# Kernel optimization log

Measured on AMD Instinct MI355X. Metric: run time of the kernel, lower is better.

## Reference

```python
import jax, jax.numpy as jnp
import numpy as np

N = 65536            # total nodes = B * NODES_PER_GRAPH
E = 524288           # edges (avg degree 8)
B = 64               # graphs per batch
NODES_PER_GRAPH = 1024
KS = 3               # SplineConv kernel_size per pseudo-dim
DEG = 2              # B-spline degree


def setup_inputs() -> dict:
    key = jax.random.key(0)
    ks = jax.random.split(key, 32)

    def w(k, shape, fan_in):
        return jax.random.normal(k, shape, jnp.float32) * (1.0 / np.sqrt(fan_in))

    inp = {
        "x": jax.random.normal(ks[0], (N, 16), jnp.float32),
        "edge_index": jax.random.randint(ks[1], (2, E), 0, N, jnp.int64),
        "pos": jax.random.uniform(ks[2], (E, 2), jnp.float32),  # pseudo-coords in [0,1]
        "batch": jnp.sort(jax.random.randint(ks[3], (N,), 0, B, jnp.int64)),
    }
    dims = [("enc0", 16, 32), ("enc1", 32, 64), ("enc2", 64, 64),
            ("dec0", 128, 64), ("dec1", 96, 32)]
    for i, (name, ci, co) in enumerate(dims):
        inp[name + "_W"] = w(ks[4 + 3 * i], (KS * KS, ci, co), ci * KS * KS)
        inp[name + "_root"] = w(ks[5 + 3 * i], (ci, co), ci)
        inp[name + "_b"] = jnp.zeros((co,), jnp.float32)
    inp["lin1_W"] = w(ks[20], (NODES_PER_GRAPH * 32, 128), NODES_PER_GRAPH * 32)
    inp["lin1_b"] = jnp.zeros((128,), jnp.float32)
    inp["lin2_W"] = w(ks[21], (128, 3), 128)
    inp["lin2_b"] = jnp.zeros((3,), jnp.float32)
    return inp


def _spline_basis(pseudo):
    """Open B-spline basis, degree 2, kernel_size 3, dim 2 (torch_spline_conv math).
    Returns basis [E, 9] and flattened weight indices [E, 9]."""
    v = pseudo * (KS - DEG)                    # scale to [0, ks-deg] = [0, 1]
    f = v - jnp.floor(v)                       # fractional part [E, 2]
    base = jnp.floor(v).astype(jnp.int32)
    # quadratic B-spline pieces for offsets s = 0, 1, 2
    b = jnp.stack([0.5 * (1.0 - f) ** 2, -f * f + f + 0.5, 0.5 * f * f], axis=-1)  # [E,2,3]
    idx = jnp.clip(base[..., None] + jnp.arange(3), 0, KS - 1)                      # [E,2,3]
    basis = (b[:, 0, :, None] * b[:, 1, None, :]).reshape(-1, 9)                    # [E,9]
    widx = (idx[:, 0, :, None] + KS * idx[:, 1, None, :]).reshape(-1, 9)            # [E,9]
    return basis, widx


def _spline_conv(x, src, dst, basis, widx, W, root, bias, n):
    """SplineConv: per-node transform under each of K kernels, then edge-wise
    basis-weighted gather, mean-scatter to targets, plus root linear + bias."""
    xW = jnp.einsum('ni,kio->nko', x, W)       # [N, 9, out]
    msg = basis[:, 0:1] * xW[src, widx[:, 0]]
    for s in range(1, 9):                      # fixed S = (deg+1)^2 = 9 taps
        msg = msg + basis[:, s:s + 1] * xW[src, widx[:, s]]
    agg = jax.ops.segment_sum(msg, dst, num_segments=n)
    deg = jax.ops.segment_sum(jnp.ones((msg.shape[0],), msg.dtype), dst, num_segments=n)
    out = agg / jnp.maximum(deg, 1.0)[:, None]  # mean aggregation (PyG default)
    return out + x @ root + bias


def _relu6(x):
    return jnp.clip(x, 0.0, 6.0)


def reference(x, edge_index, pos, batch,
              enc0_W, enc0_root, enc0_b,
              enc1_W, enc1_root, enc1_b,
              enc2_W, enc2_root, enc2_b,
              dec0_W, dec0_root, dec0_b,
              dec1_W, dec1_root, dec1_b,
              lin1_W, lin1_b, lin2_W, lin2_b):
    src, dst = edge_index[0], edge_index[1]
    basis, widx = _spline_basis(pos)
    n = x.shape[0]
    outs = [x]
    for W, R, bb in [(enc0_W, enc0_root, enc0_b),
                     (enc1_W, enc1_root, enc1_b),
                     (enc2_W, enc2_root, enc2_b)]:
        outs.append(_relu6(_spline_conv(outs[-1], src, dst, basis, widx, W, R, bb, n)))
    # decoder with skip-concat (encoder_bn/decoder_bn are never used in forward)
    d_in = jnp.concatenate([outs[3], outs[2]], axis=1)                 # 64+64 = 128
    dout = _relu6(_spline_conv(d_in, src, dst, basis, widx, dec0_W, dec0_root, dec0_b, n))
    d_in = jnp.concatenate([dout, outs[1]], axis=1)                    # 64+32 = 96
    dout = _relu6(_spline_conv(d_in, src, dst, basis, widx, dec1_W, dec1_root, dec1_b, n))
    flat = dout.reshape(B, NODES_PER_GRAPH * 32)                       # batch_size = max(batch)+1 = 64 (static)
    h = jax.nn.relu(flat @ lin1_W + lin1_b)
    return h @ lin2_W + lin2_b
```

## Files before the change

kernel.cpp:

```cpp
#include <hip/hip_runtime.h>

#define KS 3
#define NN 65536
#define EE 524288
#define BB 64

typedef unsigned short u16;
typedef unsigned int u32;

typedef __attribute__((ext_vector_type(8))) short bf16x8;
typedef __attribute__((ext_vector_type(4))) float f32x4;

__device__ __forceinline__ float bf2f(u16 u) {
  union { u32 i; float f; } v; v.i = ((u32)u) << 16; return v.f;
}
__device__ __forceinline__ u16 f2bf(float f) {
  union { float f; u32 i; } v; v.f = f;
  u32 x = v.i;
  x += 0x7fffu + ((x >> 16) & 1u);
  return (u16)(x >> 16);
}

static const size_t O_CR   = 0;
static const size_t O_ROWS = 10485760;
static const size_t O_CURS = 10748160;
static const size_t O_BSUM = 11010304;
static const size_t O_BMAT = 11011328;
static const size_t O_XB   = 11379968;
static const size_t O_H1   = 13477184;
static const size_t O_H2   = 17671488;
static const size_t O_H3   = 26060096;
static const size_t O_D0   = 34448704;
static const size_t O_D1   = 42837312;
static const size_t O_HBUF = 47031616;
static const size_t O_DEG  = 47064384;

__global__ void cvt_x(const float* __restrict__ x, u16* __restrict__ xb) {
  int i = blockIdx.x * 256 + threadIdx.x;
  xb[i] = f2bf(x[i]);
}

__global__ void hist_kernel(const int* __restrict__ ei, int* __restrict__ deg) {
  int e = blockIdx.x * 256 + threadIdx.x;
  int d = ei[EE + e]; d = min(max(d, 0), NN - 1);
  atomicAdd(&deg[d], 1);
}

__global__ void scan1(const int* __restrict__ deg, int* __restrict__ rows,
                      int* __restrict__ bsum) {
  __shared__ int s[256];
  int t = threadIdx.x, b = blockIdx.x, i = b * 256 + t;
  int v = deg[i];
  s[t] = v; __syncthreads();
  for (int off = 1; off < 256; off <<= 1) {
    int x = (t >= off) ? s[t - off] : 0; __syncthreads();
    s[t] += x; __syncthreads();
  }
  rows[i] = s[t] - v;
  if (t == 255) bsum[b] = s[255];
}
__global__ void scan2(int* __restrict__ bsum) {
  __shared__ int s[256];
  int t = threadIdx.x;
  int v = bsum[t];
  s[t] = v; __syncthreads();
  for (int off = 1; off < 256; off <<= 1) {
    int x = (t >= off) ? s[t - off] : 0; __syncthreads();
    s[t] += x; __syncthreads();
  }
  bsum[t] = s[t] - v;
}
__global__ void scan3(int* __restrict__ rows, const int* __restrict__ bsum,
                      int* __restrict__ cursor) {
  int t = threadIdx.x, b = blockIdx.x, i = b * 256 + t;
  int v = rows[i] + bsum[b];
  rows[i] = v;
  cursor[i] = v;
  if (i == NN - 1) rows[NN] = EE;
}

__global__ void fill_kernel(const int* __restrict__ ei, const float* __restrict__ pos,
                            int* __restrict__ cursor, u32* __restrict__ cr) {
  int e = blockIdx.x * 256 + threadIdx.x;
  int src = ei[e];      src = min(max(src, 0), NN - 1);
  int dst = ei[EE + e]; dst = min(max(dst, 0), NN - 1);
  float2 p = ((const float2*)pos)[e];
  float fl0 = floorf(p.x), fl1 = floorf(p.y);
  float f0 = p.x - fl0, f1 = p.y - fl1;
  int b0 = (int)fl0, b1 = (int)fl1;
  float w0[3] = { 0.5f*(1.f-f0)*(1.f-f0), -f0*f0+f0+0.5f, 0.5f*f0*f0 };
  float w1[3] = { 0.5f*(1.f-f1)*(1.f-f1), -f1*f1+f1+0.5f, 0.5f*f1*f1 };
  int i0[3], i1[3];
#pragma unroll
  for (int s = 0; s < 3; ++s) {
    i0[s] = min(max(b0 + s, 0), KS - 1);
    i1[s] = min(max(b1 + s, 0), KS - 1);
  }
  float c[9] = {0,0,0,0,0,0,0,0,0};
#pragma unroll
  for (int s0 = 0; s0 < 3; ++s0)
#pragma unroll
    for (int s1 = 0; s1 < 3; ++s1)
      c[i0[s0] + KS * i1[s1]] += w0[s0] * w1[s1];
  u16 h[9];
#pragma unroll
  for (int k = 0; k < 9; ++k) h[k] = f2bf(c[k]);
  int slot = atomicAdd(&cursor[dst], 1);
  slot = min(max(slot, 0), EE - 1);
  size_t b = (size_t)slot * 5;
  cr[b + 0] = (u32)(u16)src | ((u32)h[0] << 16);
  cr[b + 1] = (u32)h[1] | ((u32)h[2] << 16);
  cr[b + 2] = (u32)h[3] | ((u32)h[4] << 16);
  cr[b + 3] = (u32)h[5] | ((u32)h[6] << 16);
  cr[b + 4] = (u32)h[7] | ((u32)h[8] << 16);
}

struct BDesc { const float* W; int dstOff, i0, INW, OUT, K, isRoot; };
struct BDescs { BDesc d[18]; };

__global__ void build_b(BDescs ds, u16* __restrict__ bmat) {
  BDesc d = ds.d[blockIdx.y];
  int idx = blockIdx.x * 256 + threadIdx.x;
  int elems = d.K * d.OUT;
  if (idx >= elems) return;
  int o = idx / d.K, r = idx - o * d.K;
  float v;
  if (d.isRoot) {
    v = (r < d.INW) ? d.W[(size_t)(d.i0 + r) * d.OUT + o] : 0.f;
  } else {
    int kk = r >> 5, ii = r & 31;
    int i = d.i0 + ii;
    v = (i < d.INW) ? d.W[((size_t)kk * d.INW + i) * d.OUT + o] : 0.f;
  }
  bmat[(size_t)d.dstOff + (size_t)o * d.K + r] = f2bf(v);
}

struct PD { const u16* src; const u16* src2; int IN, IN2, mode, bOffA, ncA, bOffB, ncB; };
struct RD { const u16* src; int astride, ksteps, bOff; };
struct FArgs { PD ch; RD rt[2]; int nrt; const float* bias; u16* dst; };

#define NSTRIDE 1192

#define DECODE9U(Q0)                                              \
    u32 q1 = __builtin_amdgcn_readfirstlane(p[1]);                \
    u32 q2 = __builtin_amdgcn_readfirstlane(p[2]);                \
    u32 q3 = __builtin_amdgcn_readfirstlane(p[3]);                \
    u32 q4 = __builtin_amdgcn_readfirstlane(p[4]);                \
    float c0 = bf2f((u16)((Q0) >> 16));                           \
    float c1 = bf2f((u16)(q1 & 0xffffu)), c2 = bf2f((u16)(q1 >> 16)); \
    float c3 = bf2f((u16)(q2 & 0xffffu)), c4 = bf2f((u16)(q2 >> 16)); \
    float c5 = bf2f((u16)(q3 & 0xffffu)), c6 = bf2f((u16)(q3 >> 16)); \
    float c7 = bf2f((u16)(q4 & 0xffffu)), c8 = bf2f((u16)(q4 >> 16));

#define DECODE9V(Q0)                                              \
    u32 q1 = p[1], q2 = p[2], q3 = p[3], q4 = p[4];               \
    float c0 = bf2f((u16)((Q0) >> 16));                           \
    float c1 = bf2f((u16)(q1 & 0xffffu)), c2 = bf2f((u16)(q1 >> 16)); \
    float c3 = bf2f((u16)(q2 & 0xffffu)), c4 = bf2f((u16)(q2 >> 16)); \
    float c5 = bf2f((u16)(q3 & 0xffffu)), c6 = bf2f((u16)(q3 >> 16)); \
    float c7 = bf2f((u16)(q4 & 0xffffu)), c8 = bf2f((u16)(q4 >> 16));

#define ACC9(DST, XV) do {                                        \
    DST[0] = fmaf(c0, (XV), DST[0]); DST[1] = fmaf(c1, (XV), DST[1]); \
    DST[2] = fmaf(c2, (XV), DST[2]); DST[3] = fmaf(c3, (XV), DST[3]); \
    DST[4] = fmaf(c4, (XV), DST[4]); DST[5] = fmaf(c5, (XV), DST[5]); \
    DST[6] = fmaf(c6, (XV), DST[6]); DST[7] = fmaf(c7, (XV), DST[7]); \
    DST[8] = fmaf(c8, (XV), DST[8]); } while (0)

template <int OUT>
__global__ __launch_bounds__(256, 8) void fused_layer(FArgs fa, const u32* __restrict__ cr,
                                                      const int* __restrict__ rows,
                                                      const u16* __restrict__ bmat) {
  __shared__ u16 aggl[8 * NSTRIDE];
  constexpr int NT = OUT / 16;
  const int tid = threadIdx.x;
  const int wave = tid >> 6, lane = tid & 63;
  const int quad = lane >> 4, l16 = lane & 15;
  const int l = lane & 31, half = lane >> 5;
  const int nb = blockIdx.x * 8;

  const PD d = fa.ch;
  if (d.mode == 0) {
    const bool has2 = d.src2 != nullptr;
    const bool v2 = has2 && (lane < d.IN2);
    const u16* sp  = d.src + lane;
    const u16* sp2 = has2 ? d.src2 + (v2 ? lane : 0) : nullptr;
    const int st2 = d.IN2;
    const int cslot  = half * 296 + l;
    const int cslotB = 2 * 296 + half * 296 + l;
    for (int nn = 0; nn < 2; ++nn) {
      const int node = nb + wave * 2 + nn;
      const int rs = rows[node], re = rows[node + 1];
      float a[9] = {0,0,0,0,0,0,0,0,0};
      float b9[9] = {0,0,0,0,0,0,0,0,0};
      int r = rs;
      for (; r + 3 < re; r += 4) {
        u32 w0[4]; float xv[4], yv[4];
#pragma unroll
        for (int g = 0; g < 4; ++g) w0[g] = cr[(size_t)(r + g) * 5];
#pragma unroll
        for (int g = 0; g < 4; ++g)
          xv[g] = bf2f(sp[(size_t)(w0[g] & 0xffffu) * 64]);
        if (has2) {
#pragma unroll
          for (int g = 0; g < 4; ++g)
            yv[g] = v2 ? bf2f(sp2[(size_t)(w0[g] & 0xffffu) * st2]) : 0.f;
        }
#pragma unroll
        for (int g = 0; g < 4; ++g) {
          const u32* p = cr + (size_t)(r + g) * 5;
          u32 q0 = __builtin_amdgcn_readfirstlane(w0[g]);
          DECODE9U(q0);
          ACC9(a, xv[g]);
          if (has2) ACC9(b9, yv[g]);
        }
      }
      for (; r < re; ++r) {
        const u32* p = cr + (size_t)r * 5;
        u32 w0 = p[0];
        float xv = bf2f(sp[(size_t)(w0 & 0xffffu) * 64]);
        float yv = 0.f;
        if (has2) yv = v2 ? bf2f(sp2[(size_t)(w0 & 0xffffu) * st2]) : 0.f;
        u32 q0 = __builtin_amdgcn_readfirstlane(w0);
        DECODE9U(q0);
        ACC9(a, xv);
        if (has2) ACC9(b9, yv);
      }
      const float inv = 1.f / fmaxf((float)(re - rs), 1.f);
      const int row = wave * 2 + nn;
#pragma unroll
      for (int k = 0; k < 9; ++k)
        aggl[row * NSTRIDE + cslot + k * 32] = f2bf(a[k] * inv);
      if (has2) {
#pragma unroll
        for (int k = 0; k < 9; ++k)
          aggl[row * NSTRIDE + cslotB + k * 32] = f2bf(b9[k] * inv);
      }
    }
  } else {
    const int i = l;
    const bool valid = i < d.IN;
    const u16* sp = d.src + i;
    const int IN = d.IN;
    for (int nn = 0; nn < 2; ++nn) {
      const int node = nb + wave * 2 + nn;
      const int rs = rows[node], re = rows[node + 1];
      float a[9] = {0,0,0,0,0,0,0,0,0};
      int r = rs + half;
      for (; r + 2 < re; r += 4) {
        u32 w0[2]; float xv[2];
#pragma unroll
        for (int g = 0; g < 2; ++g) w0[g] = cr[(size_t)(r + 2 * g) * 5];
#pragma unroll
        for (int g = 0; g < 2; ++g)
          xv[g] = valid ? bf2f(sp[(size_t)(w0[g] & 0xffffu) * IN]) : 0.f;
#pragma unroll
        for (int g = 0; g < 2; ++g) {
          const u32* p = cr + (size_t)(r + 2 * g) * 5;
          u32 q0 = w0[g];
          DECODE9V(q0);
          ACC9(a, xv[g]);
        }
      }
      for (; r < re; r += 2) {
        const u32* p = cr + (size_t)r * 5;
        u32 q0 = p[0];
        float xv = valid ? bf2f(sp[(size_t)(q0 & 0xffffu) * IN]) : 0.f;
        DECODE9V(q0);
        ACC9(a, xv);
      }
#pragma unroll
      for (int k = 0; k < 9; ++k) a[k] += __shfl_xor(a[k], 32);
      const float inv = 1.f / fmaxf((float)(re - rs), 1.f);
      if (half == 0) {
#pragma unroll
        for (int k = 0; k < 9; ++k)
          aggl[(wave * 2 + nn) * NSTRIDE + k * 32 + l] = f2bf(a[k] * inv);
      }
    }
  }
  __syncthreads();

  if (wave < NT) {
    f32x4 C = (f32x4){0.f, 0.f, 0.f, 0.f};
    for (int cc = 0; cc < d.ncA; ++cc) {
      const u16* Bp = bmat + d.bOffA + cc * 288 * OUT;
      for (int ks = 0; ks < 9; ++ks) {
        bf16x8 av = *(const bf16x8*)&aggl[l16 * NSTRIDE + cc * 296 + ks * 32 + quad * 8];
        bf16x8 bv = *(const bf16x8*)(Bp + ((size_t)(wave * 16 + l16) * 9 + ks) * 32 + quad * 8);
        C = __builtin_amdgcn_mfma_f32_16x16x32_bf16(av, bv, C, 0, 0, 0);
      }
    }
    for (int cc = 0; cc < d.ncB; ++cc) {
      const u16* Bp = bmat + d.bOffB + cc * 288 * OUT;
      for (int ks = 0; ks < 9; ++ks) {
        bf16x8 av = *(const bf16x8*)&aggl[l16 * NSTRIDE + (2 + cc) * 296 + ks * 32 + quad * 8];
        bf16x8 bv = *(const bf16x8*)(Bp + ((size_t)(wave * 16 + l16) * 9 + ks) * 32 + quad * 8);
        C = __builtin_amdgcn_mfma_f32_16x16x32_bf16(av, bv, C, 0, 0, 0);
      }
    }
    for (int rx = 0; rx < fa.nrt; ++rx) {
      const RD rd = fa.rt[rx];
      for (int ks = 0; ks < rd.ksteps; ++ks) {
        bf16x8 av = *(const bf16x8*)(rd.src + (size_t)(nb + l16) * rd.astride + ks * 32 + quad * 8);
        bf16x8 bv = *(const bf16x8*)(bmat + rd.bOff
                     + ((size_t)(wave * 16 + l16) * rd.ksteps + ks) * 32 + quad * 8);
        C = __builtin_amdgcn_mfma_f32_16x16x32_bf16(av, bv, C, 0, 0, 0);
      }
    }
    if (quad < 2) {
#pragma unroll
      for (int r = 0; r < 4; ++r) {
        int node = nb + quad * 4 + r;
        int o = wave * 16 + l16;
        float v = C[r] + fa.bias[o];
        v = fminf(fmaxf(v, 0.f), 6.f);
        fa.dst[(size_t)node * OUT + o] = f2bf(v);
      }
    }
  }
}

__global__ __launch_bounds__(256) void mlp1(const u16* __restrict__ d1,
                                            const float* __restrict__ w1,
                                            float* __restrict__ hbuf) {
  __shared__ __align__(16) u16 bt[128 * 136];
  const int tid = threadIdx.x;
  const int c0 = blockIdx.x * 128;
  for (int idx = tid; idx < 16384; idx += 256) {
    int k = idx >> 7, col = idx & 127;
    bt[col * 136 + k] = f2bf(w1[(size_t)(c0 + k) * 128 + col]);
  }
  __syncthreads();
  const int wave = tid >> 6, lane = tid & 63;
  const int quad = lane >> 4, l16 = lane & 15;
  f32x4 C[8];
#pragma unroll
  for (int nt = 0; nt < 8; ++nt) C[nt] = (f32x4){0.f, 0.f, 0.f, 0.f};
  for (int ks = 0; ks < 4; ++ks) {
    bf16x8 av = *(const bf16x8*)(d1 + (size_t)(wave * 16 + l16) * 32768 + c0 + ks * 32 + quad * 8);
#pragma unroll
    for (int nt = 0; nt < 8; ++nt) {
      bf16x8 bv = *(const bf16x8*)&bt[(nt * 16 + l16) * 136 + ks * 32 + quad * 8];
      C[nt] = __builtin_amdgcn_mfma_f32_16x16x32_bf16(av, bv, C[nt], 0, 0, 0);
    }
  }
#pragma unroll
  for (int nt = 0; nt < 8; ++nt)
#pragma unroll
    for (int r = 0; r < 4; ++r) {
      int g = wave * 16 + quad * 4 + r;
      int o = nt * 16 + l16;
      atomicAdd(&hbuf[g * 128 + o], C[nt][r]);
    }
}

__global__ void mlp2(const float* __restrict__ hbuf, const float* __restrict__ b1,
                     const float* __restrict__ w2, const float* __restrict__ b2,
                     float* __restrict__ out) {
  const int t = threadIdx.x;
  if (t >= BB * 3) return;
  const int g = t / 3, c = t % 3;
  float acc = b2[c];
  for (int j = 0; j < 128; ++j) {
    float h = fmaxf(hbuf[g * 128 + j] + b1[j], 0.f);
    acc = fmaf(h, w2[j * 3 + c], acc);
  }
  out[g * 3 + c] = acc;
}

extern "C" void kernel_launch(void* const* d_in, const int* in_sizes, int n_in,
                              void* d_out, int out_size, void* d_ws, size_t ws_size,
                              hipStream_t stream) {
  const float* x   = (const float*)d_in[0];
  const int*   ei  = (const int*)d_in[1];
  const float* pos = (const float*)d_in[2];

  char* base = (char*)d_ws;
  u32*   cr     = (u32*)(base + O_CR);
  int*   rows   = (int*)(base + O_ROWS);
  int*   cursor = (int*)(base + O_CURS);
  int*   bsum   = (int*)(base + O_BSUM);
  u16*   bmat   = (u16*)(base + O_BMAT);
  u16*   xb     = (u16*)(base + O_XB);
  u16*   h1     = (u16*)(base + O_H1);
  u16*   h2     = (u16*)(base + O_H2);
  u16*   h3     = (u16*)(base + O_H3);
  u16*   d0     = (u16*)(base + O_D0);
  u16*   d1     = (u16*)(base + O_D1);
  float* hbuf   = (float*)(base + O_HBUF);
  int*   deg    = (int*)(base + O_DEG);

  hipMemsetAsync(base + O_HBUF, 0, 32768 + 262144, stream);

  cvt_x<<<NN * 16 / 256, 256, 0, stream>>>(x, xb);
  hist_kernel<<<EE / 256, 256, 0, stream>>>(ei, deg);
  scan1<<<256, 256, 0, stream>>>(deg, rows, bsum);
  scan2<<<1, 256, 0, stream>>>(bsum);
  scan3<<<256, 256, 0, stream>>>(rows, bsum, cursor);
  fill_kernel<<<EE / 256, 256, 0, stream>>>(ei, pos, cursor, cr);

  const float* W_e0 = (const float*)d_in[4];
  const float* R_e0 = (const float*)d_in[5];
  const float* B_e0 = (const float*)d_in[6];
  const float* W_e1 = (const float*)d_in[7];
  const float* R_e1 = (const float*)d_in[8];
  const float* B_e1 = (const float*)d_in[9];
  const float* W_e2 = (const float*)d_in[10];
  const float* R_e2 = (const float*)d_in[11];
  const float* B_e2 = (const float*)d_in[12];
  const float* W_d0 = (const float*)d_in[13];
  const float* R_d0 = (const float*)d_in[14];
  const float* B_d0 = (const float*)d_in[15];
  const float* W_d1 = (const float*)d_in[16];
  const float* R_d1 = (const float*)d_in[17];
  const float* B_d1 = (const float*)d_in[18];

  BDescs ds;
  ds.d[0]  = { W_e0, 0,      0,  16,  32, 288, 0 };
  ds.d[1]  = { W_e1, 9216,   0,  32,  64, 288, 0 };
  ds.d[2]  = { W_e2, 27648,  0,  64,  64, 288, 0 };
  ds.d[3]  = { W_e2, 46080,  32, 64,  64, 288, 0 };
  ds.d[4]  = { W_d0, 64512,  0,  128, 64, 288, 0 };
  ds.d[5]  = { W_d0, 82944,  32, 128, 64, 288, 0 };
  ds.d[6]  = { W_d0, 101376, 64, 128, 64, 288, 0 };
  ds.d[7]  = { W_d0, 119808, 96, 128, 64, 288, 0 };
  ds.d[8]  = { W_d1, 138240, 0,  96,  32, 288, 0 };
  ds.d[9]  = { W_d1, 147456, 32, 96,  32, 288, 0 };
  ds.d[10] = { W_d1, 156672, 64, 96,  32, 288, 0 };
  ds.d[11] = { R_e0, 165888, 0,  16, 32, 32, 1 };
  ds.d[12] = { R_e1, 166912, 0,  32, 64, 32, 1 };
  ds.d[13] = { R_e2, 168960, 0,  64, 64, 64, 1 };
  ds.d[14] = { R_d0, 173056, 0,  64, 64, 64, 1 };
  ds.d[15] = { R_d0, 177152, 64, 64, 64, 64, 1 };
  ds.d[16] = { R_d1, 181248, 0,  64, 32, 64, 1 };
  ds.d[17] = { R_d1, 183296, 64, 32, 32, 32, 1 };
  build_b<<<dim3(72, 18), 256, 0, stream>>>(ds, bmat);

  const int FG = NN / 8;

  FArgs fe0 = { {xb, nullptr, 16, 0, 1, 0, 1, 0, 0},
                { {xb, 16, 1, 165888}, {} }, 1, B_e0, h1 };
  fused_layer<32><<<FG, 256, 0, stream>>>(fe0, cr, rows, bmat);

  FArgs fe1 = { {h1, nullptr, 32, 0, 1, 9216, 1, 0, 0},
                { {h1, 32, 1, 166912}, {} }, 1, B_e1, h2 };
  fused_layer<64><<<FG, 256, 0, stream>>>(fe1, cr, rows, bmat);

  FArgs fe2 = { {h2, nullptr, 64, 0, 0, 27648, 2, 0, 0},
                { {h2, 64, 2, 168960}, {} }, 1, B_e2, h3 };
  fused_layer<64><<<FG, 256, 0, stream>>>(fe2, cr, rows, bmat);

  FArgs fd0 = { {h3, h2, 64, 64, 0, 64512, 2, 101376, 2},
                { {h3, 64, 2, 173056}, {h2, 64, 2, 177152} }, 2, B_d0, d0 };
  fused_layer<64><<<FG, 256, 0, stream>>>(fd0, cr, rows, bmat);

  FArgs fd1 = { {d0, h1, 64, 32, 0, 138240, 2, 156672, 1},
                { {d0, 64, 2, 181248}, {h1, 32, 1, 183296} }, 2, B_d1, d1 };
  fused_layer<32><<<FG, 256, 0, stream>>>(fd1, cr, rows, bmat);

  mlp1<<<256, 256, 0, stream>>>(d1, (const float*)d_in[19], hbuf);
  mlp2<<<1, 256, 0, stream>>>(hbuf, (const float*)d_in[20], (const float*)d_in[21],
                              (const float*)d_in[22], (float*)d_out);
}
```

Measured before the change: 649.0 us.

## Reuse enc2 aggregated h2 features in dec0 instead of re-gathering

The enc2 layer now writes its per-node aggregated (edge-weighted, mean-normalised) h2 features to a workspace buffer. dec0 no longer re-gathers h2 over the edges. It treats that stored aggregate as an extra dense input, multiplied through a repacked 576-wide weight block. This removes a second gather pass over all edges for the skip-connection half, at the cost of writing and re-reading a 576-element bf16 row per node.

```diff
diff --git a/kernel.cpp b/kernel.cpp
--- a/kernel.cpp
+++ b/kernel.cpp
@@ -34,6 +34,7 @@
 static const size_t O_D1   = 42837312;
 static const size_t O_HBUF = 47031616;
 static const size_t O_DEG  = 47064384;
+static const size_t O_AGG2 = 47326528;
 
 __global__ void cvt_x(const float* __restrict__ x, u16* __restrict__ xb) {
   int i = blockIdx.x * 256 + threadIdx.x;
@@ -115,8 +116,8 @@
   cr[b + 4] = (u32)h[7] | ((u32)h[8] << 16);
 }
 
-struct BDesc { const float* W; int dstOff, i0, INW, OUT, K, isRoot; };
-struct BDescs { BDesc d[18]; };
+struct BDesc { const float* W; int dstOff, i0, INW, OUT, K, type; };
+struct BDescs { BDesc d[17]; };
 
 __global__ void build_b(BDescs ds, u16* __restrict__ bmat) {
   BDesc d = ds.d[blockIdx.y];
@@ -125,8 +126,13 @@
   if (idx >= elems) return;
   int o = idx / d.K, r = idx - o * d.K;
   float v;
-  if (d.isRoot) {
+  if (d.type == 1) {
     v = (r < d.INW) ? d.W[(size_t)(d.i0 + r) * d.OUT + o] : 0.f;
+  } else if (d.type == 2) {
+    int cc = r / 288, rem = r - cc * 288;
+    int kk = rem >> 5, ii = rem & 31;
+    int i = d.i0 + cc * 32 + ii;
+    v = d.W[((size_t)kk * d.INW + i) * d.OUT + o];
   } else {
     int kk = r >> 5, ii = r & 31;
     int i = d.i0 + ii;
@@ -137,7 +143,7 @@
 
 struct PD { const u16* src; const u16* src2; int IN, IN2, mode, bOffA, ncA, bOffB, ncB; };
 struct RD { const u16* src; int astride, ksteps, bOff; };
-struct FArgs { PD ch; RD rt[2]; int nrt; const float* bias; u16* dst; };
+struct FArgs { PD ch; RD rt[3]; int nrt; const float* bias; u16* dst; u16* aggOut; };
 
 #define NSTRIDE 1192
 
@@ -281,6 +287,22 @@
   }
   __syncthreads();
 
+  if (fa.aggOut) {
+    u32* dstw = (u32*)fa.aggOut;
+#pragma unroll
+    for (int it = 0; it < 9; ++it) {
+      int idx = it * 256 + tid;
+      int node = idx / 288;
+      int e = idx - node * 288;
+      int w = 2 * e;
+      int chunk = (w >= 288) ? 1 : 0;
+      int wc = w - chunk * 288;
+      int k = wc >> 5, ll = wc & 31;
+      u32 v = *(const u32*)&aggl[node * NSTRIDE + chunk * 296 + k * 32 + ll];
+      dstw[(size_t)(nb + node) * 288 + e] = v;
+    }
+  }
+
   if (wave < NT) {
     f32x4 C = (f32x4){0.f, 0.f, 0.f, 0.f};
     for (int cc = 0; cc < d.ncA; ++cc) {
@@ -390,6 +412,7 @@
   u16*   d1     = (u16*)(base + O_D1);
   float* hbuf   = (float*)(base + O_HBUF);
   int*   deg    = (int*)(base + O_DEG);
+  u16*   agg2   = (u16*)(base + O_AGG2);
 
   hipMemsetAsync(base + O_HBUF, 0, 32768 + 262144, stream);
 
@@ -423,40 +446,40 @@
   ds.d[3]  = { W_e2, 46080,  32, 64,  64, 288, 0 };
   ds.d[4]  = { W_d0, 64512,  0,  128, 64, 288, 0 };
   ds.d[5]  = { W_d0, 82944,  32, 128, 64, 288, 0 };
-  ds.d[6]  = { W_d0, 101376, 64, 128, 64, 288, 0 };
-  ds.d[7]  = { W_d0, 119808, 96, 128, 64, 288, 0 };
-  ds.d[8]  = { W_d1, 138240, 0,  96,  32, 288, 0 };
-  ds.d[9]  = { W_d1, 147456, 32, 96,  32, 288, 0 };
-  ds.d[10] = { W_d1, 156672, 64, 96,  32, 288, 0 };
-  ds.d[11] = { R_e0, 165888, 0,  16, 32, 32, 1 };
-  ds.d[12] = { R_e1, 166912, 0,  32, 64, 32, 1 };
-  ds.d[13] = { R_e2, 168960, 0,  64, 64, 64, 1 };
-  ds.d[14] = { R_d0, 173056, 0,  64, 64, 64, 1 };
-  ds.d[15] = { R_d0, 177152, 64, 64, 64, 64, 1 };
-  ds.d[16] = { R_d1, 181248, 0,  64, 32, 64, 1 };
-  ds.d[17] = { R_d1, 183296, 64, 32, 32, 32, 1 };
-  build_b<<<dim3(72, 18), 256, 0, stream>>>(ds, bmat);
+  ds.d[6]  = { W_d0, 101376, 64, 128, 64, 576, 2 };
+  ds.d[7]  = { W_d1, 138240, 0,  96,  32, 288, 0 };
+  ds.d[8]  = { W_d1, 147456, 32, 96,  32, 288, 0 };
+  ds.d[9]  = { W_d1, 156672, 64, 96,  32, 288, 0 };
+  ds.d[10] = { R_e0, 165888, 0,  16, 32, 32, 1 };
+  ds.d[11] = { R_e1, 166912, 0,  32, 64, 32, 1 };
+  ds.d[12] = { R_e2, 168960, 0,  64, 64, 64, 1 };
+  ds.d[13] = { R_d0, 173056, 0,  64, 64, 64, 1 };
+  ds.d[14] = { R_d0, 177152, 64, 64, 64, 64, 1 };
+  ds.d[15] = { R_d1, 181248, 0,  64, 32, 64, 1 };
+  ds.d[16] = { R_d1, 183296, 64, 32, 32, 32, 1 };
+  build_b<<<dim3(144, 17), 256, 0, stream>>>(ds, bmat);
 
   const int FG = NN / 8;
 
   FArgs fe0 = { {xb, nullptr, 16, 0, 1, 0, 1, 0, 0},
-                { {xb, 16, 1, 165888}, {} }, 1, B_e0, h1 };
+                { {xb, 16, 1, 165888}, {}, {} }, 1, B_e0, h1, nullptr };
   fused_layer<32><<<FG, 256, 0, stream>>>(fe0, cr, rows, bmat);
 
   FArgs fe1 = { {h1, nullptr, 32, 0, 1, 9216, 1, 0, 0},
-                { {h1, 32, 1, 166912}, {} }, 1, B_e1, h2 };
+                { {h1, 32, 1, 166912}, {}, {} }, 1, B_e1, h2, nullptr };
   fused_layer<64><<<FG, 256, 0, stream>>>(fe1, cr, rows, bmat);
 
   FArgs fe2 = { {h2, nullptr, 64, 0, 0, 27648, 2, 0, 0},
-                { {h2, 64, 2, 168960}, {} }, 1, B_e2, h3 };
+                { {h2, 64, 2, 168960}, {}, {} }, 1, B_e2, h3, agg2 };
   fused_layer<64><<<FG, 256, 0, stream>>>(fe2, cr, rows, bmat);
 
-  FArgs fd0 = { {h3, h2, 64, 64, 0, 64512, 2, 101376, 2},
-                { {h3, 64, 2, 173056}, {h2, 64, 2, 177152} }, 2, B_d0, d0 };
+  FArgs fd0 = { {h3, nullptr, 64, 0, 0, 64512, 2, 0, 0},
+                { {agg2, 576, 18, 101376}, {h3, 64, 2, 173056}, {h2, 64, 2, 177152} },
+                3, B_d0, d0, nullptr };
   fused_layer<64><<<FG, 256, 0, stream>>>(fd0, cr, rows, bmat);
 
   FArgs fd1 = { {d0, h1, 64, 32, 0, 138240, 2, 156672, 1},
-                { {d0, 64, 2, 181248}, {h1, 32, 1, 183296} }, 2, B_d1, d1 };
+                { {d0, 64, 2, 181248}, {h1, 32, 1, 183296}, {} }, 2, B_d1, d1, nullptr };
   fused_layer<32><<<FG, 256, 0, stream>>>(fd1, cr, rows, bmat);
 
   mlp1<<<256, 256, 0, stream>>>(d1, (const float*)d_in[19], hbuf);
```

After: 733.8 us. 13.1% more time.

## Reuse encoder edge aggregates to precompute decoder skip-branch partial outputs

Applied to the files above, without the earlier changes.

The encoder layers enc1 and enc2 already aggregate h1 and h2 over each node's edges in shared memory. They now also multiply those aggregates by the decoder weight slices for the skip inputs and write fp32 partial sums to new workspace buffers. dec0 and dec1 then gather edges only for their primary input and add the stored partials before bias and relu6. This removes the second edge gather of h2 and h1 in the decoder layers. The cost is extra MFMA work in the encoders and an fp32 partial-buffer write and read per node.

```diff
diff --git a/kernel.cpp b/kernel.cpp
--- a/kernel.cpp
+++ b/kernel.cpp
@@ -34,6 +34,8 @@
 static const size_t O_D1   = 42837312;
 static const size_t O_HBUF = 47031616;
 static const size_t O_DEG  = 47064384;
+static const size_t O_PD0  = 47326528;
+static const size_t O_PD1  = 64103744;
 
 __global__ void cvt_x(const float* __restrict__ x, u16* __restrict__ xb) {
   int i = blockIdx.x * 256 + threadIdx.x;
@@ -137,7 +139,8 @@
 
 struct PD { const u16* src; const u16* src2; int IN, IN2, mode, bOffA, ncA, bOffB, ncB; };
 struct RD { const u16* src; int astride, ksteps, bOff; };
-struct FArgs { PD ch; RD rt[2]; int nrt; const float* bias; u16* dst; };
+struct FArgs { PD ch; RD rt[2]; int nrt; const float* bias; u16* dst;
+               const float* pin; float* pout; int poutW, pBOffA, pncA; };
 
 #define NSTRIDE 1192
 
@@ -281,6 +284,23 @@
   }
   __syncthreads();
 
+  if (fa.pout && wave < (fa.poutW >> 4)) {
+    f32x4 P = (f32x4){0.f, 0.f, 0.f, 0.f};
+    for (int cc = 0; cc < fa.pncA; ++cc) {
+      const u16* Bp = bmat + fa.pBOffA + cc * 288 * fa.poutW;
+      for (int ks = 0; ks < 9; ++ks) {
+        bf16x8 av = *(const bf16x8*)&aggl[l16 * NSTRIDE + cc * 296 + ks * 32 + quad * 8];
+        bf16x8 bv = *(const bf16x8*)(Bp + ((size_t)(wave * 16 + l16) * 9 + ks) * 32 + quad * 8);
+        P = __builtin_amdgcn_mfma_f32_16x16x32_bf16(av, bv, P, 0, 0, 0);
+      }
+    }
+    if (quad < 2) {
+#pragma unroll
+      for (int r = 0; r < 4; ++r)
+        fa.pout[(size_t)(nb + quad * 4 + r) * fa.poutW + wave * 16 + l16] = P[r];
+    }
+  }
+
   if (wave < NT) {
     f32x4 C = (f32x4){0.f, 0.f, 0.f, 0.f};
     for (int cc = 0; cc < d.ncA; ++cc) {
@@ -314,6 +334,7 @@
         int node = nb + quad * 4 + r;
         int o = wave * 16 + l16;
         float v = C[r] + fa.bias[o];
+        if (fa.pin) v += fa.pin[(size_t)node * OUT + o];
         v = fminf(fmaxf(v, 0.f), 6.f);
         fa.dst[(size_t)node * OUT + o] = f2bf(v);
       }
@@ -390,6 +411,8 @@
   u16*   d1     = (u16*)(base + O_D1);
   float* hbuf   = (float*)(base + O_HBUF);
   int*   deg    = (int*)(base + O_DEG);
+  float* pd0    = (float*)(base + O_PD0);
+  float* pd1    = (float*)(base + O_PD1);
 
   hipMemsetAsync(base + O_HBUF, 0, 32768 + 262144, stream);
 
@@ -440,23 +463,28 @@
   const int FG = NN / 8;
 
   FArgs fe0 = { {xb, nullptr, 16, 0, 1, 0, 1, 0, 0},
-                { {xb, 16, 1, 165888}, {} }, 1, B_e0, h1 };
+                { {xb, 16, 1, 165888}, {} }, 1, B_e0, h1,
+                nullptr, nullptr, 0, 0, 0 };
   fused_layer<32><<<FG, 256, 0, stream>>>(fe0, cr, rows, bmat);
 
   FArgs fe1 = { {h1, nullptr, 32, 0, 1, 9216, 1, 0, 0},
-                { {h1, 32, 1, 166912}, {} }, 1, B_e1, h2 };
+                { {h1, 32, 1, 166912}, {} }, 1, B_e1, h2,
+                nullptr, pd1, 32, 156672, 1 };
   fused_layer<64><<<FG, 256, 0, stream>>>(fe1, cr, rows, bmat);
 
   FArgs fe2 = { {h2, nullptr, 64, 0, 0, 27648, 2, 0, 0},
-                { {h2, 64, 2, 168960}, {} }, 1, B_e2, h3 };
+                { {h2, 64, 2, 168960}, {} }, 1, B_e2, h3,
+                nullptr, pd0, 64, 101376, 2 };
   fused_layer<64><<<FG, 256, 0, stream>>>(fe2, cr, rows, bmat);
 
-  FArgs fd0 = { {h3, h2, 64, 64, 0, 64512, 2, 101376, 2},
-                { {h3, 64, 2, 173056}, {h2, 64, 2, 177152} }, 2, B_d0, d0 };
+  FArgs fd0 = { {h3, nullptr, 64, 0, 0, 64512, 2, 0, 0},
+                { {h3, 64, 2, 173056}, {h2, 64, 2, 177152} }, 2, B_d0, d0,
+                pd0, nullptr, 0, 0, 0 };
   fused_layer<64><<<FG, 256, 0, stream>>>(fd0, cr, rows, bmat);
 
-  FArgs fd1 = { {d0, h1, 64, 32, 0, 138240, 2, 156672, 1},
-                { {d0, 64, 2, 181248}, {h1, 32, 1, 183296} }, 2, B_d1, d1 };
+  FArgs fd1 = { {d0, nullptr, 64, 0, 0, 138240, 2, 0, 0},
+                { {d0, 64, 2, 181248}, {h1, 32, 1, 183296} }, 2, B_d1, d1,
+                pd1, nullptr, 0, 0, 0 };
   fused_layer<32><<<FG, 256, 0, stream>>>(fd1, cr, rows, bmat);
 
   mlp1<<<256, 256, 0, stream>>>(d1, (const float*)d_in[19], hbuf);
```

After: 614.5 us. 1.06x faster.
